# Optimization experiments

Hardware: AMD Instinct MI355X
Metric: run time of the kernel (lower is better)

The kernel has to match this reference:

```python
import jax, jax.numpy as jnp
import numpy as np

R = 8          # num_real
P = 8          # num_complex_conjugate_pairs
L = 4          # num_layers (hidden Linear+ReLU blocks)
H = 256        # hidden_dim
B = 16384      # batch


def _init_params(key, C, out_dim):
    ks = jax.random.split(key, 6)
    s_in = 1.0  # fan_in = 1
    s_h = 1.0 / np.sqrt(H)
    return dict(
        W_in=jax.random.uniform(ks[0], (C, H), jnp.float32, -s_in, s_in),
        b_in=jax.random.uniform(ks[1], (C, H), jnp.float32, -s_in, s_in),
        W_h=jax.random.uniform(ks[2], (L, C, H, H), jnp.float32, -s_h, s_h),
        b_h=jax.random.uniform(ks[3], (L, C, H), jnp.float32, -s_h, s_h),
        W_out=jax.random.uniform(ks[4], (C, out_dim, H), jnp.float32, -s_h, s_h),
        b_out=jax.random.uniform(ks[5], (C, out_dim), jnp.float32, -s_h, s_h),
    )


def setup_inputs() -> dict:
    key = jax.random.key(0)
    kz, kr, kc = jax.random.split(key, 3)
    z = jax.random.normal(kz, (B, R + 2 * P), jnp.float32)
    pr = _init_params(kr, R, 1)   # real-eigenvalue MLPs, out_dim=1
    pc = _init_params(kc, P, 2)   # complex-pair MLPs, out_dim=2
    return {
        "z": z,
        "Wr_in": pr["W_in"], "br_in": pr["b_in"],
        "Wr_h": pr["W_h"], "br_h": pr["b_h"],
        "Wr_out": pr["W_out"], "br_out": pr["b_out"],
        "Wc_in": pc["W_in"], "bc_in": pc["b_in"],
        "Wc_h": pc["W_h"], "bc_h": pc["b_h"],
        "Wc_out": pc["W_out"], "bc_out": pc["b_out"],
    }


def _grouped_mlp(x, W_in, b_in, W_h, b_h, W_out, b_out):
    # x: [B, C] scalar input per channel; all C tiny MLPs run as grouped GEMMs.
    h = jax.nn.relu(x[..., None] * W_in + b_in)            # [B, C, H]
    for l in range(W_h.shape[0]):
        h = jax.nn.relu(jnp.einsum('bci,coi->bco', h, W_h[l]) + b_h[l])
    return jnp.einsum('bci,coi->bco', h, W_out) + b_out     # [B, C, out]


def reference(z, Wr_in, br_in, Wr_h, br_h, Wr_out, br_out,
              Wc_in, bc_in, Wc_h, bc_h, Wc_out, bc_out):
    # real channels: z[..., i] -> Linear chains -> real_lambda [B, R]
    real_lambda = _grouped_mlp(z[..., :R], Wr_in, br_in, Wr_h, br_h,
                               Wr_out, br_out)[..., 0]
    # complex pairs: magnitude z_r^2 + z_i^2 per pair -> (mu, omega)
    z_mag = z[..., R::2] ** 2 + z[..., R + 1::2] ** 2        # [B, P]
    mu_omega = _grouped_mlp(z_mag, Wc_in, bc_in, Wc_h, bc_h,
                            Wc_out, bc_out)                  # [B, P, 2]
    mu = mu_omega[..., 0]
    omega = mu_omega[..., 1]
    return real_lambda, mu, omega
```

## Files before the change

kernel.cpp:

```cpp
#include <hip/hip_runtime.h>

#define OUT_MU 131072
#define OUT_OM 262144
#define BIAS_OFF 4194304
#define WOUT_OFF 4210688

typedef _Float16 half8 __attribute__((ext_vector_type(8)));
typedef _Float16 half4 __attribute__((ext_vector_type(4)));
typedef float    floatx4 __attribute__((ext_vector_type(4)));

__device__ __forceinline__ void wait_lgkm0() {
    asm volatile("s_waitcnt lgkmcnt(0)" ::: "memory");
}
__device__ __forceinline__ void barrier_raw() {
    asm volatile("s_barrier" ::: "memory");
}

__global__ void prep_w(const float* __restrict__ Wr_h,
                       const float* __restrict__ Wc_h,
                       _Float16* __restrict__ dst) {
    int v = blockIdx.x * 256 + threadIdx.x;
    int r16 = v & 15;
    int ks  = (v >> 4) & 3;
    int nt  = (v >> 6) & 3;
    int wv  = (v >> 8) & 3;
    int g   = (v >> 10) & 31;
    int ch  = v >> 15;
    int l = g >> 3, kk = g & 7;
    int n  = wv * 64 + nt * 16 + r16;
    int k0 = kk * 32 + ks * 8;
    const float* src = (ch < 8) ? Wr_h : Wc_h;
    int c = ch & 7;
    const float* p = src + ((size_t)((l * 8 + c) * 256 + n)) * 256 + k0;
    float4 a = *(const float4*)p;
    float4 b = *(const float4*)(p + 4);
    half8 o;
    o[0] = (_Float16)a.x; o[1] = (_Float16)a.y; o[2] = (_Float16)a.z; o[3] = (_Float16)a.w;
    o[4] = (_Float16)b.x; o[5] = (_Float16)b.y; o[6] = (_Float16)b.z; o[7] = (_Float16)b.w;
    *(half8*)(dst + (size_t)v * 8) = o;
}

__global__ void prep_b(const float* __restrict__ br_h,
                       const float* __restrict__ bc_h,
                       _Float16* __restrict__ dst) {
    int t = blockIdx.x * 256 + threadIdx.x;
    int idx = t & 63, blk = t >> 6;
    int rq = blk & 3, wv = (blk >> 2) & 3, ch = blk >> 4;
    int j = idx >> 3, rem = idx & 7;
    int l = j >> 1, nthi = j & 1;
    int ntlo = rem >> 2, e = rem & 3;
    int nt = nthi * 2 + ntlo;
    int n = wv * 64 + nt * 16 + rq * 4 + e;
    const float* src = (ch < 8) ? br_h : bc_h;
    dst[BIAS_OFF + t] = (_Float16)src[(l * 8 + (ch & 7)) * 256 + n];
}

__global__ void prep_wo(const float* __restrict__ Wr_out,
                        const float* __restrict__ Wc_out,
                        _Float16* __restrict__ dst) {
    int t = blockIdx.x * 256 + threadIdx.x;
    int j = t & 255, d = (t >> 8) & 1, ch = t >> 9;
    int c = ch & 7;
    float v;
    if (ch < 8) v = d ? 0.f : Wr_out[c * 256 + j];
    else        v = Wc_out[(c * 2 + d) * 256 + j];
    dst[WOUT_OFF + t] = (_Float16)v;
}

__global__ __launch_bounds__(256, 2)
void mlp_fused(const float* __restrict__ z,
               const float* __restrict__ Wr_in, const float* __restrict__ br_in,
               const float* __restrict__ Wc_in, const float* __restrict__ bc_in,
               const float* __restrict__ br_out, const float* __restrict__ bc_out,
               const _Float16* __restrict__ wst,
               float* __restrict__ out) {
    __shared__ __align__(16) char smem[65536];
    const int tid  = threadIdx.x;
    const int lane = tid & 63;
    const int wv   = tid >> 6;
    const int bid  = blockIdx.x;
    const int ch   = bid & 15;
    const int m0   = (bid >> 4) * 128;
    const bool isC = ch >= 8;
    const int c    = ch & 7;
    const int ks   = lane >> 4;
    const int r16  = lane & 15;

    const half8* wl = (const half8*)wst + (size_t)ch * 32768 + wv * 256 + lane;
    const half8* bp = (const half8*)(wst + BIAS_OFF) + (((ch * 4 + wv) * 4 + ks) * 8);

    half8 wr[2][4];
    #pragma unroll
    for (int nt = 0; nt < 4; ++nt) wr[0][nt] = wl[nt * 64];

    int vb[8];
    #pragma unroll
    for (int mt = 0; mt < 8; ++mt)
        vb[mt] = (mt * 16 + r16) * 512 + (((r16 & 7) ^ ks) << 4);

    {
        const int jg = tid & 31;
        const int rg = tid >> 5;
        const float* Wi = (isC ? Wc_in : Wr_in) + c * 256 + jg * 8;
        const float* bi = (isC ? bc_in : br_in) + c * 256 + jg * 8;
        float4 w0 = *(const float4*)Wi;
        float4 w1 = *(const float4*)(Wi + 4);
        float4 v0 = *(const float4*)bi;
        float4 v1 = *(const float4*)(bi + 4);
        #pragma unroll
        for (int i = 0; i < 16; ++i) {
            int m = rg * 16 + i;
            const float* zr = z + (size_t)(m0 + m) * 24;
            float x;
            if (!isC) x = zr[c];
            else { float a = zr[8 + 2 * c], b = zr[9 + 2 * c]; x = a * a + b * b; }
            half8 o;
            o[0] = (_Float16)fmaxf(fmaf(x, w0.x, v0.x), 0.f);
            o[1] = (_Float16)fmaxf(fmaf(x, w0.y, v0.y), 0.f);
            o[2] = (_Float16)fmaxf(fmaf(x, w0.z, v0.z), 0.f);
            o[3] = (_Float16)fmaxf(fmaf(x, w0.w, v0.w), 0.f);
            o[4] = (_Float16)fmaxf(fmaf(x, w1.x, v1.x), 0.f);
            o[5] = (_Float16)fmaxf(fmaf(x, w1.y, v1.y), 0.f);
            o[6] = (_Float16)fmaxf(fmaf(x, w1.z, v1.z), 0.f);
            o[7] = (_Float16)fmaxf(fmaf(x, w1.w, v1.w), 0.f);
            *(half8*)(smem + m * 512 + ((jg ^ (m & 7)) << 4)) = o;
        }
    }
    wait_lgkm0();
    barrier_raw();

    #pragma unroll 1
    for (int l = 0; l < 4; ++l) {
        half8 bl0 = bp[l * 2], bl1 = bp[l * 2 + 1];

        floatx4 acc[4][8];
        #pragma unroll
        for (int a = 0; a < 4; ++a)
            #pragma unroll
            for (int b = 0; b < 8; ++b) acc[a][b] = 0.f;

        half8 bfr[2][4];
        #pragma unroll
        for (int j = 0; j < 4; ++j)
            bfr[0][j] = *(const half8*)(smem + vb[j]);

        #pragma unroll
        for (int hs = 0; hs < 16; ++hs) {
            const int kk = hs >> 1, half = hs & 1;
            if (half == 0) {
                const half8* p = wl + (kk + 1) * 1024;
                #pragma unroll
                for (int nt = 0; nt < 4; ++nt) wr[(kk + 1) & 1][nt] = p[nt * 64];
            }
            if (hs < 15) {
                const int nkk = (hs + 1) >> 1, nhalf = (hs + 1) & 1;
                #pragma unroll
                for (int j = 0; j < 4; ++j)
                    bfr[nhalf][j] = *(const half8*)(smem + (vb[nhalf * 4 + j] ^ (nkk << 6)));
            }
            __builtin_amdgcn_s_setprio(1);
            #pragma unroll
            for (int nt = 0; nt < 4; ++nt)
                #pragma unroll
                for (int j = 0; j < 4; ++j)
                    acc[nt][half * 4 + j] = __builtin_amdgcn_mfma_f32_16x16x32_f16(
                        wr[kk & 1][nt], bfr[half][j], acc[nt][half * 4 + j], 0, 0, 0);
            __builtin_amdgcn_s_setprio(0);
        }
        wl += 8192;

        wait_lgkm0();
        barrier_raw();
        #pragma unroll
        for (int nt = 0; nt < 4; ++nt) {
            const int nb = wv * 64 + nt * 16 + ks * 4;
            half8 bv = (nt < 2) ? bl0 : bl1;
            float b0 = (float)bv[(nt & 1) * 4 + 0];
            float b1 = (float)bv[(nt & 1) * 4 + 1];
            float b2 = (float)bv[(nt & 1) * 4 + 2];
            float b3 = (float)bv[(nt & 1) * 4 + 3];
            #pragma unroll
            for (int mt = 0; mt < 8; ++mt) {
                const int m = mt * 16 + r16;
                floatx4 v = acc[nt][mt];
                half4 o;
                o[0] = (_Float16)fmaxf(v[0] + b0, 0.f);
                o[1] = (_Float16)fmaxf(v[1] + b1, 0.f);
                o[2] = (_Float16)fmaxf(v[2] + b2, 0.f);
                o[3] = (_Float16)fmaxf(v[3] + b3, 0.f);
                *(half4*)(smem + m * 512 + (((nb >> 3) ^ (m & 7)) << 4) + (nb & 7) * 2) = o;
            }
        }
        wait_lgkm0();
        barrier_raw();
    }

    {
        const int q = tid & 1, m = tid >> 1;
        const half8* Wo = (const half8*)(wst + WOUT_OFF) + ch * 64 + q * 16;
        float s0 = 0.f, s1 = 0.f;
        #pragma unroll
        for (int i = 0; i < 16; ++i) {
            int slot = q * 16 + i;
            half8 hv = *(const half8*)(smem + m * 512 + ((slot ^ (m & 7)) << 4));
            half8 w0 = Wo[i];
            #pragma unroll
            for (int e = 0; e < 8; ++e) s0 = fmaf((float)hv[e], (float)w0[e], s0);
            if (isC) {
                half8 w1 = Wo[32 + i];
                #pragma unroll
                for (int e = 0; e < 8; ++e) s1 = fmaf((float)hv[e], (float)w1[e], s1);
            }
        }
        s0 += __shfl_xor(s0, 1);
        if (isC) s1 += __shfl_xor(s1, 1);
        if (q == 0) {
            const int row = m0 + m;
            if (!isC) {
                out[row * 8 + c] = s0 + br_out[c];
            } else {
                out[OUT_MU + row * 8 + c] = s0 + bc_out[c * 2];
                out[OUT_OM + row * 8 + c] = s1 + bc_out[c * 2 + 1];
            }
        }
    }
}

extern "C" void kernel_launch(void* const* d_in, const int* in_sizes, int n_in,
                              void* d_out, int out_size, void* d_ws, size_t ws_size,
                              hipStream_t stream) {
    const float* z      = (const float*)d_in[0];
    const float* Wr_in  = (const float*)d_in[1];
    const float* br_in  = (const float*)d_in[2];
    const float* Wr_h   = (const float*)d_in[3];
    const float* br_h   = (const float*)d_in[4];
    const float* Wr_out = (const float*)d_in[5];
    const float* br_out = (const float*)d_in[6];
    const float* Wc_in  = (const float*)d_in[7];
    const float* bc_in  = (const float*)d_in[8];
    const float* Wc_h   = (const float*)d_in[9];
    const float* bc_h   = (const float*)d_in[10];
    const float* Wc_out = (const float*)d_in[11];
    const float* bc_out = (const float*)d_in[12];
    _Float16* wst = (_Float16*)d_ws;
    float* out = (float*)d_out;

    prep_w<<<2048, 256, 0, stream>>>(Wr_h, Wc_h, wst);
    prep_b<<<64, 256, 0, stream>>>(br_h, bc_h, wst);
    prep_wo<<<32, 256, 0, stream>>>(Wr_out, Wc_out, wst);
    mlp_fused<<<2048, 256, 0, stream>>>(z, Wr_in, br_in, Wc_in, bc_in,
                                        br_out, bc_out, wst, out);
}
```

Before: 138.2 us.

## Switch hidden-layer GEMMs to 32x32x16 MFMA and stage z rows via LDS

Replaces the 16x16x32 MFMA tiling with 32x32x16 MFMA instructions. The weight prep, bias prep, LDS read swizzle and epilogue writeback are all rewritten to match the new fragment layout, so fewer, larger MFMA ops and fewer LDS fragment reads are issued per k-step. It also loads the block's z rows into extra LDS with global_load_lds instead of scattered per-thread global loads. This raises shared memory per block to 76 KB, which may reduce occupancy, and changes register pressure.

```diff
diff --git a/kernel.cpp b/kernel.cpp
--- a/kernel.cpp
+++ b/kernel.cpp
@@ -7,28 +7,33 @@
 
 typedef _Float16 half8 __attribute__((ext_vector_type(8)));
 typedef _Float16 half4 __attribute__((ext_vector_type(4)));
-typedef float    floatx4 __attribute__((ext_vector_type(4)));
+typedef float    floatx16 __attribute__((ext_vector_type(16)));
 
 __device__ __forceinline__ void wait_lgkm0() {
     asm volatile("s_waitcnt lgkmcnt(0)" ::: "memory");
 }
+__device__ __forceinline__ void wait_vm0() {
+    asm volatile("s_waitcnt vmcnt(0)" ::: "memory");
+}
 __device__ __forceinline__ void barrier_raw() {
     asm volatile("s_barrier" ::: "memory");
 }
+
+#define AS1 __attribute__((address_space(1)))
+#define AS3 __attribute__((address_space(3)))
 
 __global__ void prep_w(const float* __restrict__ Wr_h,
                        const float* __restrict__ Wc_h,
                        _Float16* __restrict__ dst) {
     int v = blockIdx.x * 256 + threadIdx.x;
-    int r16 = v & 15;
-    int ks  = (v >> 4) & 3;
-    int nt  = (v >> 6) & 3;
-    int wv  = (v >> 8) & 3;
-    int g   = (v >> 10) & 31;
-    int ch  = v >> 15;
-    int l = g >> 3, kk = g & 7;
-    int n  = wv * 64 + nt * 16 + r16;
-    int k0 = kk * 32 + ks * 8;
+    int lane = v & 63;
+    int nt   = (v >> 6) & 1;
+    int wv   = (v >> 7) & 3;
+    int ks   = (v >> 9) & 15;
+    int l    = (v >> 13) & 3;
+    int ch   = v >> 15;
+    int n  = wv * 64 + nt * 32 + (lane & 31);
+    int k0 = ks * 16 + (lane >> 5) * 8;
     const float* src = (ch < 8) ? Wr_h : Wc_h;
     int c = ch & 7;
     const float* p = src + ((size_t)((l * 8 + c) * 256 + n)) * 256 + k0;
@@ -44,13 +49,14 @@
                        const float* __restrict__ bc_h,
                        _Float16* __restrict__ dst) {
     int t = blockIdx.x * 256 + threadIdx.x;
-    int idx = t & 63, blk = t >> 6;
-    int rq = blk & 3, wv = (blk >> 2) & 3, ch = blk >> 4;
-    int j = idx >> 3, rem = idx & 7;
-    int l = j >> 1, nthi = j & 1;
-    int ntlo = rem >> 2, e = rem & 3;
-    int nt = nthi * 2 + ntlo;
-    int n = wv * 64 + nt * 16 + rq * 4 + e;
+    int e  = t & 3;
+    int q  = (t >> 2) & 3;
+    int nt = (t >> 4) & 1;
+    int hi = (t >> 5) & 1;
+    int wv = (t >> 6) & 3;
+    int l  = (t >> 8) & 3;
+    int ch = (t >> 10) & 15;
+    int n = wv * 64 + nt * 32 + q * 8 + hi * 4 + e;
     const float* src = (ch < 8) ? br_h : bc_h;
     dst[BIAS_OFF + t] = (_Float16)src[(l * 8 + (ch & 7)) * 256 + n];
 }
@@ -74,7 +80,7 @@
                const float* __restrict__ br_out, const float* __restrict__ bc_out,
                const _Float16* __restrict__ wst,
                float* __restrict__ out) {
-    __shared__ __align__(16) char smem[65536];
+    __shared__ __align__(16) char smem[77824];
     const int tid  = threadIdx.x;
     const int lane = tid & 63;
     const int wv   = tid >> 6;
@@ -83,37 +89,50 @@
     const int m0   = (bid >> 4) * 128;
     const bool isC = ch >= 8;
     const int c    = ch & 7;
-    const int ks   = lane >> 4;
-    const int r16  = lane & 15;
-
-    const half8* wl = (const half8*)wst + (size_t)ch * 32768 + wv * 256 + lane;
-    const half8* bp = (const half8*)(wst + BIAS_OFF) + (((ch * 4 + wv) * 4 + ks) * 8);
-
-    half8 wr[2][4];
+    const int hi   = lane >> 5;
+    const int r32  = lane & 31;
+    float* zbuf = (float*)(smem + 65536);
+
+    {
+        const float* zs = z + (size_t)m0 * 24 + wv * 768 + lane * 4;
+        char* zd = smem + 65536 + wv * 3072;
+        __builtin_amdgcn_global_load_lds((const AS1 void*)zs,         (AS3 void*)zd,          16, 0, 0);
+        __builtin_amdgcn_global_load_lds((const AS1 void*)(zs + 256), (AS3 void*)(zd + 1024), 16, 0, 0);
+        __builtin_amdgcn_global_load_lds((const AS1 void*)(zs + 512), (AS3 void*)(zd + 2048), 16, 0, 0);
+    }
+
+    const half8* wl = (const half8*)wst + (size_t)ch * 32768 + wv * 128 + lane;
+
+    half8 wr[2][2];
     #pragma unroll
-    for (int nt = 0; nt < 4; ++nt) wr[0][nt] = wl[nt * 64];
-
-    int vb[8];
+    for (int nt = 0; nt < 2; ++nt) wr[0][nt] = wl[nt * 64];
+
+    int vb[4];
     #pragma unroll
-    for (int mt = 0; mt < 8; ++mt)
-        vb[mt] = (mt * 16 + r16) * 512 + (((r16 & 7) ^ ks) << 4);
+    for (int mt = 0; mt < 4; ++mt)
+        vb[mt] = (mt * 32 + r32) * 512 + ((hi ^ (lane & 7)) << 4);
+
+    const int jg = tid & 31;
+    const int rg = tid >> 5;
+    const float* Wi = (isC ? Wc_in : Wr_in) + c * 256 + jg * 8;
+    const float* bi = (isC ? bc_in : br_in) + c * 256 + jg * 8;
+    float4 w0 = *(const float4*)Wi;
+    float4 w1 = *(const float4*)(Wi + 4);
+    float4 v0 = *(const float4*)bi;
+    float4 v1 = *(const float4*)(bi + 4);
+
+    wait_vm0();
 
     {
-        const int jg = tid & 31;
-        const int rg = tid >> 5;
-        const float* Wi = (isC ? Wc_in : Wr_in) + c * 256 + jg * 8;
-        const float* bi = (isC ? bc_in : br_in) + c * 256 + jg * 8;
-        float4 w0 = *(const float4*)Wi;
-        float4 w1 = *(const float4*)(Wi + 4);
-        float4 v0 = *(const float4*)bi;
-        float4 v1 = *(const float4*)(bi + 4);
         #pragma unroll
         for (int i = 0; i < 16; ++i) {
             int m = rg * 16 + i;
-            const float* zr = z + (size_t)(m0 + m) * 24;
             float x;
-            if (!isC) x = zr[c];
-            else { float a = zr[8 + 2 * c], b = zr[9 + 2 * c]; x = a * a + b * b; }
+            if (!isC) x = zbuf[m * 24 + c];
+            else {
+                float2 p = *(const float2*)(zbuf + m * 24 + 8 + 2 * c);
+                x = p.x * p.x + p.y * p.y;
+            }
             half8 o;
             o[0] = (_Float16)fmaxf(fmaf(x, w0.x, v0.x), 0.f);
             o[1] = (_Float16)fmaxf(fmaf(x, w0.y, v0.y), 0.f);
@@ -129,42 +148,44 @@
     wait_lgkm0();
     barrier_raw();
 
+    const half8* bpc = (const half8*)(wst + BIAS_OFF) + ((ch * 4) * 4 + wv) * 8 + hi * 4;
+
     #pragma unroll 1
     for (int l = 0; l < 4; ++l) {
-        half8 bl0 = bp[l * 2], bl1 = bp[l * 2 + 1];
-
-        floatx4 acc[4][8];
-        #pragma unroll
-        for (int a = 0; a < 4; ++a)
-            #pragma unroll
-            for (int b = 0; b < 8; ++b) acc[a][b] = 0.f;
+        const half8* bl = bpc + l * 32;
+        half8 bb0 = bl[0], bb1 = bl[1], bb2 = bl[2], bb3 = bl[3];
+
+        floatx16 acc[2][4];
+        #pragma unroll
+        for (int a = 0; a < 2; ++a)
+            #pragma unroll
+            for (int b = 0; b < 4; ++b) acc[a][b] = 0.f;
 
         half8 bfr[2][4];
         #pragma unroll
-        for (int j = 0; j < 4; ++j)
-            bfr[0][j] = *(const half8*)(smem + vb[j]);
-
-        #pragma unroll
-        for (int hs = 0; hs < 16; ++hs) {
-            const int kk = hs >> 1, half = hs & 1;
-            if (half == 0) {
-                const half8* p = wl + (kk + 1) * 1024;
-                #pragma unroll
-                for (int nt = 0; nt < 4; ++nt) wr[(kk + 1) & 1][nt] = p[nt * 64];
-            }
-            if (hs < 15) {
-                const int nkk = (hs + 1) >> 1, nhalf = (hs + 1) & 1;
-                #pragma unroll
-                for (int j = 0; j < 4; ++j)
-                    bfr[nhalf][j] = *(const half8*)(smem + (vb[nhalf * 4 + j] ^ (nkk << 6)));
+        for (int mt = 0; mt < 4; ++mt)
+            bfr[0][mt] = *(const half8*)(smem + vb[mt]);
+
+        #pragma unroll
+        for (int ks = 0; ks < 16; ++ks) {
+            {
+                const half8* p = wl + (ks + 1) * 512;
+                wr[(ks + 1) & 1][0] = p[0];
+                wr[(ks + 1) & 1][1] = p[64];
+            }
+            if (ks < 15) {
+                #pragma unroll
+                for (int mt = 0; mt < 4; ++mt)
+                    bfr[(ks + 1) & 1][mt] =
+                        *(const half8*)(smem + (vb[mt] ^ ((ks + 1) << 5)));
             }
             __builtin_amdgcn_s_setprio(1);
             #pragma unroll
-            for (int nt = 0; nt < 4; ++nt)
-                #pragma unroll
-                for (int j = 0; j < 4; ++j)
-                    acc[nt][half * 4 + j] = __builtin_amdgcn_mfma_f32_16x16x32_f16(
-                        wr[kk & 1][nt], bfr[half][j], acc[nt][half * 4 + j], 0, 0, 0);
+            for (int nt = 0; nt < 2; ++nt)
+                #pragma unroll
+                for (int mt = 0; mt < 4; ++mt)
+                    acc[nt][mt] = __builtin_amdgcn_mfma_f32_32x32x16_f16(
+                        wr[ks & 1][nt], bfr[ks & 1][mt], acc[nt][mt], 0, 0, 0);
             __builtin_amdgcn_s_setprio(0);
         }
         wl += 8192;
@@ -172,23 +193,28 @@
         wait_lgkm0();
         barrier_raw();
         #pragma unroll
-        for (int nt = 0; nt < 4; ++nt) {
-            const int nb = wv * 64 + nt * 16 + ks * 4;
-            half8 bv = (nt < 2) ? bl0 : bl1;
-            float b0 = (float)bv[(nt & 1) * 4 + 0];
-            float b1 = (float)bv[(nt & 1) * 4 + 1];
-            float b2 = (float)bv[(nt & 1) * 4 + 2];
-            float b3 = (float)bv[(nt & 1) * 4 + 3];
-            #pragma unroll
-            for (int mt = 0; mt < 8; ++mt) {
-                const int m = mt * 16 + r16;
-                floatx4 v = acc[nt][mt];
-                half4 o;
-                o[0] = (_Float16)fmaxf(v[0] + b0, 0.f);
-                o[1] = (_Float16)fmaxf(v[1] + b1, 0.f);
-                o[2] = (_Float16)fmaxf(v[2] + b2, 0.f);
-                o[3] = (_Float16)fmaxf(v[3] + b3, 0.f);
-                *(half4*)(smem + m * 512 + (((nb >> 3) ^ (m & 7)) << 4) + (nb & 7) * 2) = o;
+        for (int nt = 0; nt < 2; ++nt) {
+            #pragma unroll
+            for (int q = 0; q < 4; ++q) {
+                half8 bv = (nt * 2 + (q >> 1)) == 0 ? bb0 :
+                           (nt * 2 + (q >> 1)) == 1 ? bb1 :
+                           (nt * 2 + (q >> 1)) == 2 ? bb2 : bb3;
+                const int be = (q & 1) * 4;
+                float b0 = (float)bv[be + 0];
+                float b1 = (float)bv[be + 1];
+                float b2 = (float)bv[be + 2];
+                float b3 = (float)bv[be + 3];
+                const int slot = wv * 8 + nt * 4 + q;
+                #pragma unroll
+                for (int mt = 0; mt < 4; ++mt) {
+                    const int m = mt * 32 + r32;
+                    half4 o;
+                    o[0] = (_Float16)fmaxf(acc[nt][mt][4 * q + 0] + b0, 0.f);
+                    o[1] = (_Float16)fmaxf(acc[nt][mt][4 * q + 1] + b1, 0.f);
+                    o[2] = (_Float16)fmaxf(acc[nt][mt][4 * q + 2] + b2, 0.f);
+                    o[3] = (_Float16)fmaxf(acc[nt][mt][4 * q + 3] + b3, 0.f);
+                    *(half4*)(smem + m * 512 + ((slot ^ (m & 7)) << 4) + hi * 8) = o;
+                }
             }
         }
         wait_lgkm0();
@@ -203,13 +229,13 @@
         for (int i = 0; i < 16; ++i) {
             int slot = q * 16 + i;
             half8 hv = *(const half8*)(smem + m * 512 + ((slot ^ (m & 7)) << 4));
-            half8 w0 = Wo[i];
-            #pragma unroll
-            for (int e = 0; e < 8; ++e) s0 = fmaf((float)hv[e], (float)w0[e], s0);
+            half8 wo0 = Wo[i];
+            #pragma unroll
+            for (int e = 0; e < 8; ++e) s0 = fmaf((float)hv[e], (float)wo0[e], s0);
             if (isC) {
-                half8 w1 = Wo[32 + i];
-                #pragma unroll
-                for (int e = 0; e < 8; ++e) s1 = fmaf((float)hv[e], (float)w1[e], s1);
+                half8 wo1 = Wo[32 + i];
+                #pragma unroll
+                for (int e = 0; e < 8; ++e) s1 = fmaf((float)hv[e], (float)wo1[e], s1);
             }
         }
         s0 += __shfl_xor(s0, 1);
```

New measurement: 146.3 us. 1.06x slower.
